# Kernel optimization log

Measured on AMD Instinct MI355X. Metric: run time of the kernel, lower is better.

The kernel has to match this reference:

```python
import jax, jax.numpy as jnp
import numpy as np

EPS = 1e-6
B, H, V, DH = 4096, 16, 8, 128


def setup_inputs() -> dict:
    key = jax.random.key(0)
    ks = jax.random.split(key, 7)
    s = 1.0 / np.sqrt(DH)  # ~ torch Linear init scale
    return {
        "iso_heads": jax.random.normal(ks[0], (B, H, DH), jnp.float32),
        "view_head_tokens": jax.random.normal(ks[1], (B, H, V, DH), jnp.float32),
        "pi": jax.random.uniform(ks[2], (B, H, V), jnp.float32),
        "Wq": jax.random.normal(ks[3], (H, DH, DH), jnp.float32) * s,
        "Wk": jax.random.normal(ks[4], (H, DH, DH), jnp.float32) * s,
        "Wv": jax.random.normal(ks[5], (H, DH, DH), jnp.float32) * s,
        "Wo": jax.random.normal(ks[6], (H, DH, DH), jnp.float32) * s,
    }


def reference(iso_heads, view_head_tokens, pi, Wq, Wk, Wv, Wo):
    # Per-head linears: torch Linear(y = x @ W.T), W stored (out, in) -> 'hed' (e=out, d=in)
    q = jnp.einsum("bhd,hed->bhe", iso_heads, Wq)            # [B,H,Dh]
    k = jnp.einsum("bhvd,hed->bhve", view_head_tokens, Wk)   # [B,H,V,Dh]
    v = jnp.einsum("bhvd,hed->bhve", view_head_tokens, Wv)   # [B,H,V,Dh]
    # Single-query attention per head with additive log-prior bias
    scores = jnp.einsum("bhd,bhvd->bhv", q, k) / jnp.sqrt(jnp.float32(DH))
    scores = scores + jnp.log(pi + EPS)
    attn = jax.nn.softmax(scores, axis=-1)                   # dropout = identity (eval)
    ctx = jnp.einsum("bhv,bhvd->bhd", attn, v)               # [B,H,Dh]
    out = jnp.einsum("bhd,hed->bhe", ctx, Wo)                # [B,H,Dh]
    return (out, attn)
```

## Files before the change

kernel.cpp:

```cpp
#include <hip/hip_runtime.h>
#include <cstdint>
#include <cstddef>

#define H_  16
#define V_  8
#define DH_ 128
#define B_  4096
#define BT  16
#define LDST 132

__global__ __launch_bounds__(256) void precompute_MN(
    const float* __restrict__ Wq, const float* __restrict__ Wk,
    const float* __restrict__ Wv, const float* __restrict__ Wo,
    float* __restrict__ Mmat, float* __restrict__ NTmat)
{
    const int bx    = blockIdx.x;
    const int which = bx & 1;
    const int h     = (bx >> 1) & 15;
    const int chunk = bx >> 5;
    const int tid   = threadIdx.x;
    const int col   = tid & 127;
    const int r     = chunk * 2 + (tid >> 7);

    float acc = 0.f;
    if (which == 0) {
        const float* wq = Wq + h * DH_ * DH_;
        const float* wk = Wk + h * DH_ * DH_;
#pragma unroll 8
        for (int e = 0; e < DH_; ++e)
            acc += wq[e * DH_ + r] * wk[e * DH_ + col];
        Mmat[h * DH_ * DH_ + (size_t)r * DH_ + col] = acc;
    } else {
        const float* wo = Wo + h * DH_ * DH_;
        const float* wv = Wv + h * DH_ * DH_;
#pragma unroll 8
        for (int d = 0; d < DH_; ++d)
            acc += wo[(size_t)r * DH_ + d] * wv[d * DH_ + col];
        NTmat[h * DH_ * DH_ + (size_t)col * DH_ + r] = acc;
    }
}

__global__ __launch_bounds__(128, 8) void fused_attn(
    const float* __restrict__ iso, const float* __restrict__ view,
    const float* __restrict__ pi,
    const float* __restrict__ Mmat, const float* __restrict__ NTmat,
    float* __restrict__ out, float* __restrict__ attn_out)
{
    __shared__ float buf_s[BT][LDST];
    __shared__ float sc_s[BT][V_];
    __shared__ float at_s[BT][V_];

    const int tid = threadIdx.x;
    const int h   = blockIdx.x >> 8;
    const int b0  = (blockIdx.x & 255) * BT;

#pragma unroll
    for (int i = 0; i < 4; ++i) {
        const int idx = tid + i * 128;
        const int b   = idx >> 5;
        const int dq  = idx & 31;
        const float4 v4 = *(const float4*)(iso + ((size_t)(b0 + b) * H_ + h) * DH_ + dq * 4);
        *(float4*)&buf_s[b][dq * 4] = v4;
    }
    __syncthreads();

    const int tx = tid & 31;
    const int ty = tid >> 5;

    float acc[4][4];

    {
        const float* Mh = Mmat + h * DH_ * DH_ + tx * 4;
#pragma unroll
        for (int i = 0; i < 4; ++i)
#pragma unroll
            for (int j = 0; j < 4; ++j) acc[i][j] = 0.f;

        for (int d = 0; d < DH_; d += 4) {
            const float4 m0 = *(const float4*)(Mh + (size_t)(d + 0) * DH_);
            const float4 m1 = *(const float4*)(Mh + (size_t)(d + 1) * DH_);
            const float4 m2 = *(const float4*)(Mh + (size_t)(d + 2) * DH_);
            const float4 m3 = *(const float4*)(Mh + (size_t)(d + 3) * DH_);
#pragma unroll
            for (int i = 0; i < 4; ++i) {
                const float4 a = *(const float4*)&buf_s[ty * 4 + i][d];
                acc[i][0] += a.x * m0.x + a.y * m1.x + a.z * m2.x + a.w * m3.x;
                acc[i][1] += a.x * m0.y + a.y * m1.y + a.z * m2.y + a.w * m3.y;
                acc[i][2] += a.x * m0.z + a.y * m1.z + a.z * m2.z + a.w * m3.z;
                acc[i][3] += a.x * m0.w + a.y * m1.w + a.z * m2.w + a.w * m3.w;
            }
        }
    }
    __syncthreads();

#pragma unroll
    for (int i = 0; i < 4; ++i)
        *(float4*)&buf_s[ty * 4 + i][tx * 4] =
            make_float4(acc[i][0], acc[i][1], acc[i][2], acc[i][3]);
    __syncthreads();

    {
        const int wv_  = tid >> 6;
        const int lane = tid & 63;
        const int half = lane >> 5;
        const int l32  = lane & 31;
#pragma unroll 4
        for (int it = 0; it < 32; ++it) {
            const int p  = wv_ * 64 + it * 2 + half;
            const int bl = p >> 3;
            const int v  = p & 7;
            const float4 w = *(const float4*)(view +
                (((size_t)(b0 + bl) * H_ + h) * V_ + v) * DH_ + l32 * 4);
            const float4 q = *(const float4*)&buf_s[bl][l32 * 4];
            float s = w.x * q.x + w.y * q.y + w.z * q.z + w.w * q.w;
            s += __shfl_xor(s, 1);
            s += __shfl_xor(s, 2);
            s += __shfl_xor(s, 4);
            s += __shfl_xor(s, 8);
            s += __shfl_xor(s, 16);
            if (l32 == 0) sc_s[bl][v] = s;
        }
    }
    __syncthreads();

    {
        const int bl = tid >> 3;
        const int v  = tid & 7;
        float sc = sc_s[bl][v] * 0.08838834764831845f;
        sc += logf(pi[((size_t)(b0 + bl) * H_ + h) * V_ + v] + 1e-6f);

        float mx = sc;
        mx = fmaxf(mx, __shfl_xor(mx, 1));
        mx = fmaxf(mx, __shfl_xor(mx, 2));
        mx = fmaxf(mx, __shfl_xor(mx, 4));
        const float ex = expf(sc - mx);
        float sm = ex;
        sm += __shfl_xor(sm, 1);
        sm += __shfl_xor(sm, 2);
        sm += __shfl_xor(sm, 4);
        const float at = ex / sm;
        at_s[bl][v] = at;
        attn_out[((size_t)(b0 + bl) * H_ + h) * V_ + v] = at;
    }
    __syncthreads();

    {
        const int bg  = tid >> 5;
        const int l32 = tid & 31;
#pragma unroll
        for (int r = 0; r < 4; ++r) {
            const int b = r * 4 + bg;
            const float* vbase = view + (((size_t)(b0 + b) * H_ + h) * V_) * DH_ + l32 * 4;
            float4 c = make_float4(0.f, 0.f, 0.f, 0.f);
#pragma unroll
            for (int vv = 0; vv < V_; ++vv) {
                const float a = at_s[b][vv];
                const float4 x = *(const float4*)(vbase + (size_t)vv * DH_);
                c.x += a * x.x; c.y += a * x.y; c.z += a * x.z; c.w += a * x.w;
            }
            *(float4*)&buf_s[b][l32 * 4] = c;
        }
    }
    __syncthreads();

    {
        const float* Nh = NTmat + h * DH_ * DH_ + tx * 4;
#pragma unroll
        for (int i = 0; i < 4; ++i)
#pragma unroll
            for (int j = 0; j < 4; ++j) acc[i][j] = 0.f;

        for (int dp = 0; dp < DH_; dp += 4) {
            const float4 n0 = *(const float4*)(Nh + (size_t)(dp + 0) * DH_);
            const float4 n1 = *(const float4*)(Nh + (size_t)(dp + 1) * DH_);
            const float4 n2 = *(const float4*)(Nh + (size_t)(dp + 2) * DH_);
            const float4 n3 = *(const float4*)(Nh + (size_t)(dp + 3) * DH_);
#pragma unroll
            for (int i = 0; i < 4; ++i) {
                const float4 a = *(const float4*)&buf_s[ty * 4 + i][dp];
                acc[i][0] += a.x * n0.x + a.y * n1.x + a.z * n2.x + a.w * n3.x;
                acc[i][1] += a.x * n0.y + a.y * n1.y + a.z * n2.y + a.w * n3.y;
                acc[i][2] += a.x * n0.z + a.y * n1.z + a.z * n2.z + a.w * n3.z;
                acc[i][3] += a.x * n0.w + a.y * n1.w + a.z * n2.w + a.w * n3.w;
            }
        }
#pragma unroll
        for (int i = 0; i < 4; ++i)
            *(float4*)(out + ((size_t)(b0 + ty * 4 + i) * H_ + h) * DH_ + tx * 4) =
                make_float4(acc[i][0], acc[i][1], acc[i][2], acc[i][3]);
    }
}

extern "C" void kernel_launch(void* const* d_in, const int* in_sizes, int n_in,
                              void* d_out, int out_size, void* d_ws, size_t ws_size,
                              hipStream_t stream)
{
    const float* iso  = (const float*)d_in[0];
    const float* view = (const float*)d_in[1];
    const float* pi   = (const float*)d_in[2];
    const float* Wq   = (const float*)d_in[3];
    const float* Wk   = (const float*)d_in[4];
    const float* Wv   = (const float*)d_in[5];
    const float* Wo   = (const float*)d_in[6];

    float* out  = (float*)d_out;
    float* attn = out + (size_t)B_ * H_ * DH_;

    float* Mmat  = (float*)d_ws;
    float* NTmat = Mmat + (size_t)H_ * DH_ * DH_;

    hipLaunchKernelGGL(precompute_MN, dim3(2048), dim3(256), 0, stream,
                       Wq, Wk, Wv, Wo, Mmat, NTmat);
    hipLaunchKernelGGL(fused_attn, dim3(H_ * (B_ / BT)), dim3(128), 0, stream,
                       iso, view, pi, Mmat, NTmat, out, attn);
}
```

Baseline: 506.9 us.

## Stage M/N weights in LDS, double batch tile, fuse scoring with softmax

The batch tile grows from 16 to 32 rows and the block from 128 to 256 threads. The per-head M and N^T matrices are now staged into shared memory in two 64-row halves, replacing the per-thread global float4 reads inside the GEMV loops. The score dot product is rewritten so 8 lanes cover one view with 16 floats each, and the softmax runs inside the same loop, which removes a shared-memory score buffer and a barrier. In exchange the kernel adds extra barriers to load the weight halves, uses about 50KB of LDS per block, and halves the grid size, which may reduce occupancy.

```diff
diff --git a/kernel.cpp b/kernel.cpp
--- a/kernel.cpp
+++ b/kernel.cpp
@@ -6,7 +6,7 @@
 #define V_  8
 #define DH_ 128
 #define B_  4096
-#define BT  16
+#define BT  32
 #define LDST 132
 
 __global__ __launch_bounds__(256) void precompute_MN(
@@ -40,155 +40,173 @@
     }
 }
 
-__global__ __launch_bounds__(128, 8) void fused_attn(
+__global__ __launch_bounds__(256, 3) void fused_attn(
     const float* __restrict__ iso, const float* __restrict__ view,
     const float* __restrict__ pi,
     const float* __restrict__ Mmat, const float* __restrict__ NTmat,
     float* __restrict__ out, float* __restrict__ attn_out)
 {
-    __shared__ float buf_s[BT][LDST];
-    __shared__ float sc_s[BT][V_];
+    __shared__ float wbuf[64 * DH_];
+    __shared__ float row_s[BT][LDST];
     __shared__ float at_s[BT][V_];
 
     const int tid = threadIdx.x;
-    const int h   = blockIdx.x >> 8;
-    const int b0  = (blockIdx.x & 255) * BT;
-
-#pragma unroll
-    for (int i = 0; i < 4; ++i) {
-        const int idx = tid + i * 128;
-        const int b   = idx >> 5;
-        const int dq  = idx & 31;
-        const float4 v4 = *(const float4*)(iso + ((size_t)(b0 + b) * H_ + h) * DH_ + dq * 4);
-        *(float4*)&buf_s[b][dq * 4] = v4;
-    }
-    __syncthreads();
+    const int h   = blockIdx.x >> 7;
+    const int b0  = (blockIdx.x & 127) * BT;
 
     const int tx = tid & 31;
     const int ty = tid >> 5;
 
+    const float* Mh = Mmat  + (size_t)h * DH_ * DH_;
+    const float* Nh = NTmat + (size_t)h * DH_ * DH_;
+
+#pragma unroll
+    for (int i = 0; i < 4; ++i) {
+        const int idx = tid + i * 256;
+        const int r   = idx >> 5;
+        const int q   = idx & 31;
+        *(float4*)&row_s[r][q * 4] =
+            *(const float4*)(iso + ((size_t)(b0 + r) * H_ + h) * DH_ + q * 4);
+    }
+#pragma unroll
+    for (int i = 0; i < 8; ++i) {
+        const int idx = tid + i * 256;
+        *(float4*)&wbuf[idx * 4] = *(const float4*)(Mh + (size_t)idx * 4);
+    }
+    __syncthreads();
+
     float acc[4][4];
-
-    {
-        const float* Mh = Mmat + h * DH_ * DH_ + tx * 4;
-#pragma unroll
-        for (int i = 0; i < 4; ++i)
-#pragma unroll
-            for (int j = 0; j < 4; ++j) acc[i][j] = 0.f;
-
-        for (int d = 0; d < DH_; d += 4) {
-            const float4 m0 = *(const float4*)(Mh + (size_t)(d + 0) * DH_);
-            const float4 m1 = *(const float4*)(Mh + (size_t)(d + 1) * DH_);
-            const float4 m2 = *(const float4*)(Mh + (size_t)(d + 2) * DH_);
-            const float4 m3 = *(const float4*)(Mh + (size_t)(d + 3) * DH_);
+#pragma unroll
+    for (int i = 0; i < 4; ++i)
+#pragma unroll
+        for (int j = 0; j < 4; ++j) acc[i][j] = 0.f;
+
+    auto mac64 = [&](int dbase) {
+#pragma unroll 4
+        for (int dd = 0; dd < 64; dd += 4) {
+            const float4 m0 = *(const float4*)&wbuf[(dd + 0) * DH_ + tx * 4];
+            const float4 m1 = *(const float4*)&wbuf[(dd + 1) * DH_ + tx * 4];
+            const float4 m2 = *(const float4*)&wbuf[(dd + 2) * DH_ + tx * 4];
+            const float4 m3 = *(const float4*)&wbuf[(dd + 3) * DH_ + tx * 4];
 #pragma unroll
             for (int i = 0; i < 4; ++i) {
-                const float4 a = *(const float4*)&buf_s[ty * 4 + i][d];
+                const float4 a = *(const float4*)&row_s[ty * 4 + i][dbase + dd];
                 acc[i][0] += a.x * m0.x + a.y * m1.x + a.z * m2.x + a.w * m3.x;
                 acc[i][1] += a.x * m0.y + a.y * m1.y + a.z * m2.y + a.w * m3.y;
                 acc[i][2] += a.x * m0.z + a.y * m1.z + a.z * m2.z + a.w * m3.z;
                 acc[i][3] += a.x * m0.w + a.y * m1.w + a.z * m2.w + a.w * m3.w;
             }
         }
-    }
-    __syncthreads();
-
-#pragma unroll
-    for (int i = 0; i < 4; ++i)
-        *(float4*)&buf_s[ty * 4 + i][tx * 4] =
+    };
+
+    mac64(0);
+    __syncthreads();
+
+#pragma unroll
+    for (int i = 0; i < 8; ++i) {
+        const int idx = tid + i * 256;
+        *(float4*)&wbuf[idx * 4] = *(const float4*)(Mh + 8192 + (size_t)idx * 4);
+    }
+    __syncthreads();
+
+    mac64(64);
+
+#pragma unroll
+    for (int i = 0; i < 4; ++i)
+        *(float4*)&row_s[ty * 4 + i][tx * 4] =
             make_float4(acc[i][0], acc[i][1], acc[i][2], acc[i][3]);
-    __syncthreads();
 
     {
-        const int wv_  = tid >> 6;
+        const int w    = tid >> 6;
         const int lane = tid & 63;
-        const int half = lane >> 5;
-        const int l32  = lane & 31;
-#pragma unroll 4
-        for (int it = 0; it < 32; ++it) {
-            const int p  = wv_ * 64 + it * 2 + half;
-            const int bl = p >> 3;
-            const int v  = p & 7;
-            const float4 w = *(const float4*)(view +
-                (((size_t)(b0 + bl) * H_ + h) * V_ + v) * DH_ + l32 * 4);
-            const float4 q = *(const float4*)&buf_s[bl][l32 * 4];
-            float s = w.x * q.x + w.y * q.y + w.z * q.z + w.w * q.w;
+        const int g    = lane >> 3;
+        const int i8   = lane & 7;
+
+        for (int r = 0; r < 8; ++r) {
+            const int row   = w * 8 + r;
+            const size_t bh = (size_t)(b0 + row) * H_ + h;
+            const float* vp = view + (bh * V_ + g) * DH_ + i8 * 16;
+            const float* qp = &row_s[row][i8 * 16];
+            const float4 x0 = *(const float4*)(vp + 0);
+            const float4 x1 = *(const float4*)(vp + 4);
+            const float4 x2 = *(const float4*)(vp + 8);
+            const float4 x3 = *(const float4*)(vp + 12);
+            const float4 q0 = *(const float4*)(qp + 0);
+            const float4 q1 = *(const float4*)(qp + 4);
+            const float4 q2 = *(const float4*)(qp + 8);
+            const float4 q3 = *(const float4*)(qp + 12);
+            float s = x0.x*q0.x + x0.y*q0.y + x0.z*q0.z + x0.w*q0.w
+                    + x1.x*q1.x + x1.y*q1.y + x1.z*q1.z + x1.w*q1.w
+                    + x2.x*q2.x + x2.y*q2.y + x2.z*q2.z + x2.w*q2.w
+                    + x3.x*q3.x + x3.y*q3.y + x3.z*q3.z + x3.w*q3.w;
             s += __shfl_xor(s, 1);
             s += __shfl_xor(s, 2);
             s += __shfl_xor(s, 4);
-            s += __shfl_xor(s, 8);
-            s += __shfl_xor(s, 16);
-            if (l32 == 0) sc_s[bl][v] = s;
-        }
-    }
-    __syncthreads();
-
-    {
-        const int bl = tid >> 3;
-        const int v  = tid & 7;
-        float sc = sc_s[bl][v] * 0.08838834764831845f;
-        sc += logf(pi[((size_t)(b0 + bl) * H_ + h) * V_ + v] + 1e-6f);
-
-        float mx = sc;
-        mx = fmaxf(mx, __shfl_xor(mx, 1));
-        mx = fmaxf(mx, __shfl_xor(mx, 2));
-        mx = fmaxf(mx, __shfl_xor(mx, 4));
-        const float ex = expf(sc - mx);
-        float sm = ex;
-        sm += __shfl_xor(sm, 1);
-        sm += __shfl_xor(sm, 2);
-        sm += __shfl_xor(sm, 4);
-        const float at = ex / sm;
-        at_s[bl][v] = at;
-        attn_out[((size_t)(b0 + bl) * H_ + h) * V_ + v] = at;
-    }
-    __syncthreads();
-
-    {
-        const int bg  = tid >> 5;
-        const int l32 = tid & 31;
-#pragma unroll
-        for (int r = 0; r < 4; ++r) {
-            const int b = r * 4 + bg;
-            const float* vbase = view + (((size_t)(b0 + b) * H_ + h) * V_) * DH_ + l32 * 4;
-            float4 c = make_float4(0.f, 0.f, 0.f, 0.f);
-#pragma unroll
-            for (int vv = 0; vv < V_; ++vv) {
-                const float a = at_s[b][vv];
-                const float4 x = *(const float4*)(vbase + (size_t)vv * DH_);
-                c.x += a * x.x; c.y += a * x.y; c.z += a * x.z; c.w += a * x.w;
-            }
-            *(float4*)&buf_s[b][l32 * 4] = c;
-        }
-    }
-    __syncthreads();
-
-    {
-        const float* Nh = NTmat + h * DH_ * DH_ + tx * 4;
-#pragma unroll
-        for (int i = 0; i < 4; ++i)
-#pragma unroll
-            for (int j = 0; j < 4; ++j) acc[i][j] = 0.f;
-
-        for (int dp = 0; dp < DH_; dp += 4) {
-            const float4 n0 = *(const float4*)(Nh + (size_t)(dp + 0) * DH_);
-            const float4 n1 = *(const float4*)(Nh + (size_t)(dp + 1) * DH_);
-            const float4 n2 = *(const float4*)(Nh + (size_t)(dp + 2) * DH_);
-            const float4 n3 = *(const float4*)(Nh + (size_t)(dp + 3) * DH_);
-#pragma unroll
-            for (int i = 0; i < 4; ++i) {
-                const float4 a = *(const float4*)&buf_s[ty * 4 + i][dp];
-                acc[i][0] += a.x * n0.x + a.y * n1.x + a.z * n2.x + a.w * n3.x;
-                acc[i][1] += a.x * n0.y + a.y * n1.y + a.z * n2.y + a.w * n3.y;
-                acc[i][2] += a.x * n0.z + a.y * n1.z + a.z * n2.z + a.w * n3.z;
-                acc[i][3] += a.x * n0.w + a.y * n1.w + a.z * n2.w + a.w * n3.w;
+            if (i8 == 0) {
+                float sc = s * 0.08838834764831845f
+                         + logf(pi[bh * V_ + g] + 1e-6f);
+                float mx = sc;
+                mx = fmaxf(mx, __shfl_xor(mx, 8));
+                mx = fmaxf(mx, __shfl_xor(mx, 16));
+                mx = fmaxf(mx, __shfl_xor(mx, 32));
+                const float ex = expf(sc - mx);
+                float den = ex;
+                den += __shfl_xor(den, 8);
+                den += __shfl_xor(den, 16);
+                den += __shfl_xor(den, 32);
+                const float at = ex / den;
+                at_s[row][g] = at;
+                attn_out[bh * V_ + g] = at;
             }
         }
-#pragma unroll
-        for (int i = 0; i < 4; ++i)
-            *(float4*)(out + ((size_t)(b0 + ty * 4 + i) * H_ + h) * DH_ + tx * 4) =
-                make_float4(acc[i][0], acc[i][1], acc[i][2], acc[i][3]);
-    }
+
+        const int half = lane >> 5;
+        const int c    = lane & 31;
+#pragma unroll
+        for (int t = 0; t < 4; ++t) {
+            const int row   = w * 8 + t * 2 + half;
+            const size_t bh = (size_t)(b0 + row) * H_ + h;
+            const float* vb = view + bh * V_ * DH_ + c * 4;
+            float4 cx = make_float4(0.f, 0.f, 0.f, 0.f);
+#pragma unroll
+            for (int v = 0; v < V_; ++v) {
+                const float a  = at_s[row][v];
+                const float4 x = *(const float4*)(vb + (size_t)v * DH_);
+                cx.x += a * x.x; cx.y += a * x.y; cx.z += a * x.z; cx.w += a * x.w;
+            }
+            *(float4*)&row_s[row][c * 4] = cx;
+        }
+    }
+    __syncthreads();
+
+#pragma unroll
+    for (int i = 0; i < 8; ++i) {
+        const int idx = tid + i * 256;
+        *(float4*)&wbuf[idx * 4] = *(const float4*)(Nh + (size_t)idx * 4);
+    }
+    __syncthreads();
+
+#pragma unroll
+    for (int i = 0; i < 4; ++i)
+#pragma unroll
+        for (int j = 0; j < 4; ++j) acc[i][j] = 0.f;
+
+    mac64(0);
+    __syncthreads();
+
+#pragma unroll
+    for (int i = 0; i < 8; ++i) {
+        const int idx = tid + i * 256;
+        *(float4*)&wbuf[idx * 4] = *(const float4*)(Nh + 8192 + (size_t)idx * 4);
+    }
+    __syncthreads();
+
+    mac64(64);
+
+#pragma unroll
+    for (int i = 0; i < 4; ++i)
+        *(float4*)(out + ((size_t)(b0 + ty * 4 + i) * H_ + h) * DH_ + tx * 4) =
+            make_float4(acc[i][0], acc[i][1], acc[i][2], acc[i][3]);
 }
 
 extern "C" void kernel_launch(void* const* d_in, const int* in_sizes, int n_in,
@@ -211,6 +229,6 @@
 
     hipLaunchKernelGGL(precompute_MN, dim3(2048), dim3(256), 0, stream,
                        Wq, Wk, Wv, Wo, Mmat, NTmat);
-    hipLaunchKernelGGL(fused_attn, dim3(H_ * (B_ / BT)), dim3(128), 0, stream,
+    hipLaunchKernelGGL(fused_attn, dim3(H_ * (B_ / BT)), dim3(256), 0, stream,
                        iso, view, pi, Mmat, NTmat, out, attn);
 }
```

Result: faster. 484.8 us (-4.4%).
